# Kernel tuning notes

Hardware: AMD Instinct MI355X
Metric: run time of the kernel (lower is better)

Reference implementation:

```python
import jax, jax.numpy as jnp
import numpy as np

B, T, D = 8, 2048, 1024
H, N = 8, 32  # n_heads, n_state


def _xavier(key, shape, fan_in, fan_out):
    lim = float(np.sqrt(6.0 / (fan_in + fan_out)))
    return jax.random.uniform(key, shape, jnp.float32, -lim, lim)


def setup_inputs() -> dict:
    key = jax.random.key(0)
    ks = jax.random.split(key, 8)
    x = jax.random.normal(ks[0], (B, T, D), jnp.float32)
    W_in = _xavier(ks[1], (D, D), D, D)                    # in_proj.weight [d_inner, dim]
    # per-head xavier on [n_state, d_inner] slices -> limit sqrt(6/(N+D))
    W_k = _xavier(ks[2], (H * N, D), N, D)
    W_v = _xavier(ks[3], (H * N, D), N, D)
    W_q = _xavier(ks[4], (H * N, D), N, D)
    W_beta = _xavier(ks[5], (H * N, D), N, D)
    b_beta = jnp.full((H, N), 2.0, jnp.float32)            # init_beta_bias
    W_out = _xavier(ks[6], (D, H * N), H * N, D)           # out_proj.weight [dim, H*n]
    return {"x": x, "W_in": W_in, "W_k": W_k, "W_v": W_v, "W_q": W_q,
            "W_beta": W_beta, "b_beta": b_beta, "W_out": W_out}


def reference(x, W_in, W_k, W_v, W_q, W_beta, b_beta, W_out):
    b, t, d = x.shape
    h, n = b_beta.shape
    # in_proj + SiLU (use_conv=False)
    xp = jax.nn.silu(jnp.einsum('btd,ed->bte', x, W_in))   # [B,T,D_inner]
    def proj(W):  # -> [T,B,H,N]
        return jnp.einsum('btd,md->btm', xp, W).reshape(b, t, h, n).transpose(1, 0, 2, 3)
    k_all = proj(W_k)
    v_all = proj(W_v)
    q_all = proj(W_q)
    beta_all = jax.nn.sigmoid(proj(W_beta) + b_beta)       # [T,B,H,N]

    S0 = jnp.zeros((b, h, n, n), x.dtype)

    def step(S, inp):
        k, v, q, beta = inp                                 # each [B,H,N]
        kn = k / (jnp.linalg.norm(k, axis=-1, keepdims=True) + 1e-6)
        retrieved = jnp.einsum('bhij,bhj->bhi', S, kn)
        delta = v - retrieved
        S = jnp.tanh(beta[..., None] * S + delta[..., None] * kn[..., None, :])
        Sq = jnp.einsum('bhij,bhj->bhi', S, q)
        out = Sq * jax.nn.silu(Sq)                          # [B,H,N]
        return S, out

    S_final, outs = jax.lax.scan(step, S0, (k_all, v_all, q_all, beta_all))
    cell_out = outs.transpose(1, 0, 2, 3).reshape(b, t, h * n)  # [B,T,H*N]
    y = jnp.einsum('btm,dm->btd', cell_out, W_out)          # out_proj, no bias
    return y, S_final
```

## Files before the change

### kernel.cpp

```cpp
#include <hip/hip_runtime.h>
#include <hip/hip_bf16.h>

#define TT 2048
#define BB 8
#define HH 8
#define NNS 32
#define MM (BB * TT)
#define CH 16

typedef __attribute__((ext_vector_type(8))) short short8;
typedef __attribute__((ext_vector_type(4))) float f32x4;

__device__ __forceinline__ float bf2f(ushort u) {
    return __uint_as_float(((unsigned)u) << 16);
}
__device__ __forceinline__ ushort f2bf(float f) {
    unsigned x = __float_as_uint(f);
    unsigned r = (x + 0x7fffu + ((x >> 16) & 1u)) >> 16;
    return (ushort)r;
}
__device__ __forceinline__ float sigmoidf_fast(float x) {
    float e = __builtin_amdgcn_exp2f(x * -1.4426950408889634f);
    return __builtin_amdgcn_rcpf(1.0f + e);
}
__device__ __forceinline__ float tanhf_fast(float x) {
    float e = __builtin_amdgcn_exp2f(x * 2.8853900817779268f);
    return fmaf(-2.0f, __builtin_amdgcn_rcpf(e + 1.0f), 1.0f);
}

template<int CTRL>
__device__ __forceinline__ float dpp_add(float x) {
    int y = __builtin_amdgcn_update_dpp(0, __float_as_int(x), CTRL, 0xF, 0xF, true);
    return x + __int_as_float(y);
}
__device__ __forceinline__ float red16(float x) {
    x = dpp_add<0xB1>(x);
    x = dpp_add<0x4E>(x);
    x = dpp_add<0x124>(x);
    x = dpp_add<0x128>(x);
    return x;
}

__device__ __forceinline__ void split8(const float4& x0, const float4& x1,
                                       ushort* __restrict__ h, ushort* __restrict__ l) {
    float xs[8] = {x0.x, x0.y, x0.z, x0.w, x1.x, x1.y, x1.z, x1.w};
#pragma unroll
    for (int i = 0; i < 8; ++i) {
        ushort hh = f2bf(xs[i]);
        h[i] = hh;
        l[i] = f2bf(xs[i] - bf2f(hh));
    }
}

__global__ __launch_bounds__(256) void conv_x_kernel(
    const float* __restrict__ src, ushort* __restrict__ hi, ushort* __restrict__ lo)
{
    size_t e = ((size_t)blockIdx.x * 256 + threadIdx.x) * 8;
    float4 x0 = *reinterpret_cast<const float4*>(src + e);
    float4 x1 = *reinterpret_cast<const float4*>(src + e + 4);
    ushort h[8], l[8];
    split8(x0, x1, h, l);
    *reinterpret_cast<uint4*>(hi + e) = *reinterpret_cast<const uint4*>(h);
    *reinterpret_cast<uint4*>(lo + e) = *reinterpret_cast<const uint4*>(l);
}

__global__ __launch_bounds__(256) void conv_w_kernel(
    const float* __restrict__ Wi, const float* __restrict__ Wk,
    const float* __restrict__ Wv, const float* __restrict__ Wq,
    const float* __restrict__ Wb, const float* __restrict__ Wo,
    ushort* __restrict__ W1h, ushort* __restrict__ W1l,
    ushort* __restrict__ W2h, ushort* __restrict__ W2l,
    ushort* __restrict__ W3h)
{
    size_t e = ((size_t)blockIdx.x * 256 + threadIdx.x) * 8;
    const float* s;
    ushort* dh; ushort* dl; size_t doff; bool dolo = true;
    if (e < 1048576) {
        s = Wi + e; dh = W1h; dl = W1l; doff = e;
    } else if (e < 2097152) {
        size_t u = e - 1048576;
        int wi = (int)(u >> 18);
        const float* sp = (wi == 0) ? Wk : (wi == 1) ? Wv : (wi == 2) ? Wq : Wb;
        s = sp + (u & 262143); dh = W2h; dl = W2l; doff = u;
    } else {
        size_t u = e - 2097152;
        s = Wo + u; dh = W3h; dl = nullptr; doff = u; dolo = false;
    }
    float4 x0 = *reinterpret_cast<const float4*>(s);
    float4 x1 = *reinterpret_cast<const float4*>(s + 4);
    ushort h[8], l[8];
    split8(x0, x1, h, l);
    *reinterpret_cast<uint4*>(dh + doff) = *reinterpret_cast<const uint4*>(h);
    if (dolo)
        *reinterpret_cast<uint4*>(dl + doff) = *reinterpret_cast<const uint4*>(l);
}

template<int ACT>
__global__ __launch_bounds__(256, 2) void gemm_planes(
    const ushort* __restrict__ Ah_g, const ushort* __restrict__ Al_g,
    const ushort* __restrict__ Wh_g, const ushort* __restrict__ Wl_g,
    const float* __restrict__ bbeta,
    ushort* __restrict__ Ch, ushort* __restrict__ Cl,
    float* __restrict__ Cf, int M, int N, int K)
{
    __shared__ __align__(16) ushort sAh[2][128][40], sAl[2][128][40];
    __shared__ __align__(16) ushort sWh[2][128][40], sWl[2][128][40];
    const int n0 = blockIdx.x * 128;
    const int m0 = blockIdx.y * 128;
    const int t  = threadIdx.x;
    const int wave = t >> 6, lane = t & 63;
    const int lr = lane & 15, lq = lane >> 4;
    const int wm = wave >> 1, wn = wave & 1;

    const int sr = t >> 1;
    const int sc = (t & 1) * 16;

    const ushort* pAh = Ah_g + (size_t)(m0 + sr) * K + sc;
    const ushort* pAl = Al_g + (size_t)(m0 + sr) * K + sc;
    const ushort* pWh = Wh_g + (size_t)(n0 + sr) * K + sc;
    const ushort* pWl = Wl_g + (size_t)(n0 + sr) * K + sc;

    f32x4 acc[4][4];
#pragma unroll
    for (int mi = 0; mi < 4; ++mi)
#pragma unroll
        for (int ni = 0; ni < 4; ++ni) acc[mi][ni] = (f32x4){0.f, 0.f, 0.f, 0.f};

    const int NK = K >> 5;

    {
        uint4 a0 = *reinterpret_cast<const uint4*>(pAh);
        uint4 a1 = *reinterpret_cast<const uint4*>(pAh + 8);
        uint4 l0 = *reinterpret_cast<const uint4*>(pAl);
        uint4 l1 = *reinterpret_cast<const uint4*>(pAl + 8);
        uint4 w0 = *reinterpret_cast<const uint4*>(pWh);
        uint4 w1 = *reinterpret_cast<const uint4*>(pWh + 8);
        uint4 u0 = *reinterpret_cast<const uint4*>(pWl);
        uint4 u1 = *reinterpret_cast<const uint4*>(pWl + 8);
        *reinterpret_cast<uint4*>(&sAh[0][sr][sc])     = a0;
        *reinterpret_cast<uint4*>(&sAh[0][sr][sc + 8]) = a1;
        *reinterpret_cast<uint4*>(&sAl[0][sr][sc])     = l0;
        *reinterpret_cast<uint4*>(&sAl[0][sr][sc + 8]) = l1;
        *reinterpret_cast<uint4*>(&sWh[0][sr][sc])     = w0;
        *reinterpret_cast<uint4*>(&sWh[0][sr][sc + 8]) = w1;
        *reinterpret_cast<uint4*>(&sWl[0][sr][sc])     = u0;
        *reinterpret_cast<uint4*>(&sWl[0][sr][sc + 8]) = u1;
    }
    __syncthreads();

    for (int ks = 0; ks < NK; ++ks) {
        const int cur = ks & 1;
        uint4 a0, a1, l0, l1, w0, w1, u0, u1;
        const bool pf = (ks + 1 < NK);
        if (pf) {
            const int off = (ks + 1) << 5;
            a0 = *reinterpret_cast<const uint4*>(pAh + off);
            a1 = *reinterpret_cast<const uint4*>(pAh + off + 8);
            l0 = *reinterpret_cast<const uint4*>(pAl + off);
            l1 = *reinterpret_cast<const uint4*>(pAl + off + 8);
            w0 = *reinterpret_cast<const uint4*>(pWh + off);
            w1 = *reinterpret_cast<const uint4*>(pWh + off + 8);
            u0 = *reinterpret_cast<const uint4*>(pWl + off);
            u1 = *reinterpret_cast<const uint4*>(pWl + off + 8);
        }
        short8 ah[4], al[4], wh[4], wl[4];
#pragma unroll
        for (int mi = 0; mi < 4; ++mi) {
            ah[mi] = *reinterpret_cast<const short8*>(&sAh[cur][wm * 64 + mi * 16 + lr][lq * 8]);
            al[mi] = *reinterpret_cast<const short8*>(&sAl[cur][wm * 64 + mi * 16 + lr][lq * 8]);
        }
#pragma unroll
        for (int ni = 0; ni < 4; ++ni) {
            wh[ni] = *reinterpret_cast<const short8*>(&sWh[cur][wn * 64 + ni * 16 + lr][lq * 8]);
            wl[ni] = *reinterpret_cast<const short8*>(&sWl[cur][wn * 64 + ni * 16 + lr][lq * 8]);
        }
#pragma unroll
        for (int mi = 0; mi < 4; ++mi) {
#pragma unroll
            for (int ni = 0; ni < 4; ++ni) {
                acc[mi][ni] = __builtin_amdgcn_mfma_f32_16x16x32_bf16(ah[mi], wh[ni], acc[mi][ni], 0, 0, 0);
                acc[mi][ni] = __builtin_amdgcn_mfma_f32_16x16x32_bf16(ah[mi], wl[ni], acc[mi][ni], 0, 0, 0);
                acc[mi][ni] = __builtin_amdgcn_mfma_f32_16x16x32_bf16(al[mi], wh[ni], acc[mi][ni], 0, 0, 0);
            }
        }
        if (pf) {
            const int nxt = cur ^ 1;
            *reinterpret_cast<uint4*>(&sAh[nxt][sr][sc])     = a0;
            *reinterpret_cast<uint4*>(&sAh[nxt][sr][sc + 8]) = a1;
            *reinterpret_cast<uint4*>(&sAl[nxt][sr][sc])     = l0;
            *reinterpret_cast<uint4*>(&sAl[nxt][sr][sc + 8]) = l1;
            *reinterpret_cast<uint4*>(&sWh[nxt][sr][sc])     = w0;
            *reinterpret_cast<uint4*>(&sWh[nxt][sr][sc + 8]) = w1;
            *reinterpret_cast<uint4*>(&sWl[nxt][sr][sc])     = u0;
            *reinterpret_cast<uint4*>(&sWl[nxt][sr][sc + 8]) = u1;
        }
        __syncthreads();
    }

#pragma unroll
    for (int mi = 0; mi < 4; ++mi) {
#pragma unroll
        for (int ni = 0; ni < 4; ++ni) {
#pragma unroll
            for (int r2 = 0; r2 < 4; ++r2) {
                int mg = m0 + wm * 64 + mi * 16 + lq * 4 + r2;
                int ng = n0 + wn * 64 + ni * 16 + lr;
                float v = acc[mi][ni][r2];
                if (ACT == 1) {
                    v = v * sigmoidf_fast(v);
                    ushort h = f2bf(v);
                    ushort lo_ = f2bf(v - bf2f(h));
                    Ch[(size_t)mg * N + ng] = h;
                    Cl[(size_t)mg * N + ng] = lo_;
                } else {
                    if (ACT == 2 && ng >= 768) v = sigmoidf_fast(v + bbeta[ng - 768]);
                    Cf[(size_t)mg * N + ng] = v;
                }
            }
        }
    }
}

__global__ __launch_bounds__(256, 2) void gemm_cell(
    const ushort* __restrict__ A, const ushort* __restrict__ Wh_g,
    float* __restrict__ C, int M, int N, int K)
{
    __shared__ __align__(16) ushort sA[2][128][40];
    __shared__ __align__(16) ushort sW[2][128][40];
    const int n0 = blockIdx.x * 128;
    const int m0 = blockIdx.y * 128;
    const int t  = threadIdx.x;
    const int wave = t >> 6, lane = t & 63;
    const int lr = lane & 15, lq = lane >> 4;
    const int wm = wave >> 1, wn = wave & 1;
    const int sr = t >> 1;
    const int sc = (t & 1) * 16;

    const ushort* pA = A    + (size_t)(m0 + sr) * K + sc;
    const ushort* pW = Wh_g + (size_t)(n0 + sr) * K + sc;

    f32x4 acc[4][4];
#pragma unroll
    for (int mi = 0; mi < 4; ++mi)
#pragma unroll
        for (int ni = 0; ni < 4; ++ni) acc[mi][ni] = (f32x4){0.f, 0.f, 0.f, 0.f};

    const int NK = K >> 5;
    {
        uint4 a0 = *reinterpret_cast<const uint4*>(pA);
        uint4 a1 = *reinterpret_cast<const uint4*>(pA + 8);
        uint4 w0 = *reinterpret_cast<const uint4*>(pW);
        uint4 w1 = *reinterpret_cast<const uint4*>(pW + 8);
        *reinterpret_cast<uint4*>(&sA[0][sr][sc])     = a0;
        *reinterpret_cast<uint4*>(&sA[0][sr][sc + 8]) = a1;
        *reinterpret_cast<uint4*>(&sW[0][sr][sc])     = w0;
        *reinterpret_cast<uint4*>(&sW[0][sr][sc + 8]) = w1;
    }
    __syncthreads();

    for (int ks = 0; ks < NK; ++ks) {
        const int cur = ks & 1;
        uint4 a0, a1, w0, w1;
        const bool pf = (ks + 1 < NK);
        if (pf) {
            const int off = (ks + 1) << 5;
            a0 = *reinterpret_cast<const uint4*>(pA + off);
            a1 = *reinterpret_cast<const uint4*>(pA + off + 8);
            w0 = *reinterpret_cast<const uint4*>(pW + off);
            w1 = *reinterpret_cast<const uint4*>(pW + off + 8);
        }
        short8 af[4], wf[4];
#pragma unroll
        for (int mi = 0; mi < 4; ++mi)
            af[mi] = *reinterpret_cast<const short8*>(&sA[cur][wm * 64 + mi * 16 + lr][lq * 8]);
#pragma unroll
        for (int ni = 0; ni < 4; ++ni)
            wf[ni] = *reinterpret_cast<const short8*>(&sW[cur][wn * 64 + ni * 16 + lr][lq * 8]);
#pragma unroll
        for (int mi = 0; mi < 4; ++mi)
#pragma unroll
            for (int ni = 0; ni < 4; ++ni)
                acc[mi][ni] = __builtin_amdgcn_mfma_f32_16x16x32_bf16(af[mi], wf[ni], acc[mi][ni], 0, 0, 0);
        if (pf) {
            const int nxt = cur ^ 1;
            *reinterpret_cast<uint4*>(&sA[nxt][sr][sc])     = a0;
            *reinterpret_cast<uint4*>(&sA[nxt][sr][sc + 8]) = a1;
            *reinterpret_cast<uint4*>(&sW[nxt][sr][sc])     = w0;
            *reinterpret_cast<uint4*>(&sW[nxt][sr][sc + 8]) = w1;
        }
        __syncthreads();
    }

#pragma unroll
    for (int mi = 0; mi < 4; ++mi) {
#pragma unroll
        for (int ni = 0; ni < 4; ++ni) {
#pragma unroll
            for (int r2 = 0; r2 < 4; ++r2) {
                int mg = m0 + wm * 64 + mi * 16 + lq * 4 + r2;
                int ng = n0 + wn * 64 + ni * 16 + lr;
                C[(size_t)mg * N + ng] = acc[mi][ni][r2];
            }
        }
    }
}

__global__ __launch_bounds__(256) void kn_kernel(
    const float* __restrict__ P, float* __restrict__ KN)
{
    int idx = blockIdx.x * 256 + threadIdx.x;
    int col = idx & 255;
    int bt  = idx >> 8;
    float k = P[(size_t)bt * 1024 + col];
    float ks = k * k;
    ks += __shfl_xor(ks, 1, 32);  ks += __shfl_xor(ks, 2, 32);
    ks += __shfl_xor(ks, 4, 32);  ks += __shfl_xor(ks, 8, 32);
    ks += __shfl_xor(ks, 16, 32);
    KN[idx] = k * __builtin_amdgcn_rcpf(sqrtf(ks) + 1e-6f);
}

__device__ __forceinline__ void lds_load8(
    float (&K_)[CH][32], float (&Q_)[CH][32], float (&VB)[CH][8],
    int base, int l, int iw,
    float (&k0)[8], float (&k1)[8], float (&q0)[8], float (&q1)[8],
    float (&vv)[8], float (&bb)[8])
{
#pragma unroll
    for (int u = 0; u < 8; ++u) {
        k0[u] = K_[base + u][l];  k1[u] = K_[base + u][l + 16];
        q0[u] = Q_[base + u][l];  q1[u] = Q_[base + u][l + 16];
        vv[u] = VB[base + u][iw]; bb[u] = VB[base + u][iw + 4];
    }
}

__device__ __forceinline__ void steps8(
    float (&k0)[8], float (&k1)[8], float (&q0)[8], float (&q1)[8],
    float (&vv)[8], float (&bb)[8],
    float& S0, float& S1, float (&sqp)[8])
{
#pragma unroll
    for (int u = 0; u < 8; ++u) {
        float p = red16(fmaf(S0, k0[u], S1 * k1[u]));
        float delta = vv[u] - p;
        S0 = tanhf_fast(fmaf(bb[u], S0, delta * k0[u]));
        S1 = tanhf_fast(fmaf(bb[u], S1, delta * k1[u]));
        sqp[u] = fmaf(S0, q0[u], S1 * q1[u]);
    }
}

__device__ __forceinline__ void flush8(
    float (&sqp)[8], ushort* __restrict__ cell, size_t crow, int l)
{
    float r0 = red16(sqp[0]), r1 = red16(sqp[1]);
    float r2 = red16(sqp[2]), r3 = red16(sqp[3]);
    float r4 = red16(sqp[4]), r5 = red16(sqp[5]);
    float r6 = red16(sqp[6]), r7 = red16(sqp[7]);
    if (l < 8) {
        float s01 = (l & 1) ? r1 : r0;
        float s23 = (l & 1) ? r3 : r2;
        float s45 = (l & 1) ? r5 : r4;
        float s67 = (l & 1) ? r7 : r6;
        float a03 = (l & 2) ? s23 : s01;
        float a47 = (l & 2) ? s67 : s45;
        float sel = (l & 4) ? a47 : a03;
        float o = sel * sel * sigmoidf_fast(sel);
        cell[crow + (size_t)l * 256] = f2bf(o);
    }
}

template<int DO_STAGE>
__device__ __forceinline__ void scan_chunk16(
    float (&K_)[CH][32], float (&Q_)[CH][32], float (&VB)[CH][8],
    float (&NK)[CH][32], float (&NQ)[CH][32], float (&NVB)[CH][8],
    const float*& gkn, const float*& gq, const float*& gv, const float*& gb,
    float (&k0A)[8], float (&k1A)[8], float (&q0A)[8], float (&q1A)[8],
    float (&vvA)[8], float (&bbA)[8],
    float (&k0B)[8], float (&k1B)[8], float (&q0B)[8], float (&q1B)[8],
    float (&vvB)[8], float (&bbB)[8],
    float& S0, float& S1, float (&sqp)[8],
    ushort* __restrict__ cell, size_t crow, int l, int iw, int j)
{
    float4 Lk0, Lk1, Lq0, Lq1;
    float Lv = 0.f, Lb = 0.f;
    if (DO_STAGE) {
        Lk0 = *reinterpret_cast<const float4*>(gkn);
        Lk1 = *reinterpret_cast<const float4*>(gkn + 8 * 256);
        Lq0 = *reinterpret_cast<const float4*>(gq);
        Lq1 = *reinterpret_cast<const float4*>(gq + 8 * 1024);
        Lv  = *gv;
        Lb  = *gb;
        gkn += CH * 256; gq += CH * 1024; gv += CH * 1024; gb += CH * 1024;
    }
    lds_load8(K_, Q_, VB, 8, l, iw, k0B, k1B, q0B, q1B, vvB, bbB);
    steps8(k0A, k1A, q0A, q1A, vvA, bbA, S0, S1, sqp);
    flush8(sqp, cell, crow, l);
    if (DO_STAGE) {
        *reinterpret_cast<float4*>(&NK[j >> 3][(j & 7) * 4]) = Lk0;
        *reinterpret_cast<float4*>(&NK[8 + (j >> 3)][(j & 7) * 4]) = Lk1;
        *reinterpret_cast<float4*>(&NQ[j >> 3][(j & 7) * 4]) = Lq0;
        *reinterpret_cast<float4*>(&NQ[8 + (j >> 3)][(j & 7) * 4]) = Lq1;
        NVB[j >> 2][j & 3] = Lv;
        NVB[j >> 2][4 + (j & 3)] = Lb;
        lds_load8(NK, NQ, NVB, 0, l, iw, k0A, k1A, q0A, q1A, vvA, bbA);
    }
    steps8(k0B, k1B, q0B, q1B, vvB, bbB, S0, S1, sqp);
    flush8(sqp, cell, crow + (size_t)8 * 256, l);
}

__global__ __launch_bounds__(64, 1) void scan_kernel(
    const float* __restrict__ P,
    const float* __restrict__ KN,
    ushort* __restrict__ cell,
    float* __restrict__ Sout)
{
    const int b    = blockIdx.x & 7;
    const int r    = blockIdx.x >> 3;
    const int h    = r & 7;
    const int quad = r >> 3;
    const int j    = threadIdx.x;
    const int l    = j & 15;
    const int iw   = j >> 4;
    const int i    = quad * 4 + iw;

    __shared__ __align__(16) float sK0[CH][32], sK1[CH][32];
    __shared__ __align__(16) float sQ0[CH][32], sQ1[CH][32];
    __shared__ __align__(16) float sVB0[CH][8], sVB1[CH][8];

    const size_t bt0 = (size_t)b * TT;
    const float* gkn = KN + (bt0 + (j >> 3)) * 256 + h * 32 + (j & 7) * 4;
    const float* gq  = P  + (bt0 + (j >> 3)) * 1024 + 512 + h * 32 + (j & 7) * 4;
    const float* gv  = P  + (bt0 + (j >> 2)) * 1024 + 256 + h * 32 + quad * 4 + (j & 3);
    const float* gb  = P  + (bt0 + (j >> 2)) * 1024 + 768 + h * 32 + quad * 4 + (j & 3);

    float k0A[8], k1A[8], q0A[8], q1A[8], vvA[8], bbA[8];
    float k0B[8], k1B[8], q0B[8], q1B[8], vvB[8], bbB[8];
    float sqp[8];
    float S0 = 0.f, S1 = 0.f;
    const size_t cb = (size_t)b * TT * 256 + h * 32 + i;

    {
        float4 K0v = *reinterpret_cast<const float4*>(gkn);
        float4 K1v = *reinterpret_cast<const float4*>(gkn + 8 * 256);
        float4 Q0v = *reinterpret_cast<const float4*>(gq);
        float4 Q1v = *reinterpret_cast<const float4*>(gq + 8 * 1024);
        float v0 = *gv, b0 = *gb;
        gkn += CH * 256; gq += CH * 1024; gv += CH * 1024; gb += CH * 1024;
        *reinterpret_cast<float4*>(&sK0[j >> 3][(j & 7) * 4]) = K0v;
        *reinterpret_cast<float4*>(&sK0[8 + (j >> 3)][(j & 7) * 4]) = K1v;
        *reinterpret_cast<float4*>(&sQ0[j >> 3][(j & 7) * 4]) = Q0v;
        *reinterpret_cast<float4*>(&sQ0[8 + (j >> 3)][(j & 7) * 4]) = Q1v;
        sVB0[j >> 2][j & 3] = v0;
        sVB0[j >> 2][4 + (j & 3)] = b0;
    }
    lds_load8(sK0, sQ0, sVB0, 0, l, iw, k0A, k1A, q0A, q1A, vvA, bbA);

    size_t crow = cb;
    for (int c = 0; c < 63; ++c) {
        scan_chunk16<1>(sK0, sQ0, sVB0, sK1, sQ1, sVB1,
                        gkn, gq, gv, gb,
                        k0A, k1A, q0A, q1A, vvA, bbA,
                        k0B, k1B, q0B, q1B, vvB, bbB,
                        S0, S1, sqp, cell, crow, l, iw, j);
        crow += (size_t)CH * 256;
        scan_chunk16<1>(sK1, sQ1, sVB1, sK0, sQ0, sVB0,
                        gkn, gq, gv, gb,
                        k0A, k1A, q0A, q1A, vvA, bbA,
                        k0B, k1B, q0B, q1B, vvB, bbB,
                        S0, S1, sqp, cell, crow, l, iw, j);
        crow += (size_t)CH * 256;
    }
    scan_chunk16<1>(sK0, sQ0, sVB0, sK1, sQ1, sVB1,
                    gkn, gq, gv, gb,
                    k0A, k1A, q0A, q1A, vvA, bbA,
                    k0B, k1B, q0B, q1B, vvB, bbB,
                    S0, S1, sqp, cell, crow, l, iw, j);
    crow += (size_t)CH * 256;
    scan_chunk16<0>(sK1, sQ1, sVB1, sK0, sQ0, sVB0,
                    gkn, gq, gv, gb,
                    k0A, k1A, q0A, q1A, vvA, bbA,
                    k0B, k1B, q0B, q1B, vvB, bbB,
                    S0, S1, sqp, cell, crow, l, iw, j);

    float* so = Sout + (((size_t)(b * HH + h)) * NNS + i) * NNS;
    so[l] = S0;
    so[l + 16] = S1;
}

extern "C" void kernel_launch(void* const* d_in, const int* in_sizes, int n_in,
                              void* d_out, int out_size, void* d_ws, size_t ws_size,
                              hipStream_t stream) {
    const float* x     = (const float*)d_in[0];
    const float* W_in  = (const float*)d_in[1];
    const float* W_k   = (const float*)d_in[2];
    const float* W_v   = (const float*)d_in[3];
    const float* W_q   = (const float*)d_in[4];
    const float* W_b   = (const float*)d_in[5];
    const float* b_b   = (const float*)d_in[6];
    const float* W_out = (const float*)d_in[7];
    float* out = (float*)d_out;

    const int M = MM;
    float* f = (float*)d_ws;
    float*  P    = f;
    ushort* Xh   = (ushort*)f;
    ushort* Xl   = Xh + (size_t)M * 1024;
    ushort* xpH  = (ushort*)(f + (size_t)M * 1024);
    ushort* xpL  = xpH + (size_t)M * 1024;
    float*  KN   = f + (size_t)2 * M * 1024;
    ushort* cell = (ushort*)(KN + (size_t)M * 256);
    ushort* wb   = cell + (size_t)M * 256;
    ushort* W1h = wb;
    ushort* W1l = W1h + 1048576;
    ushort* W2h = W1l + 1048576;
    ushort* W2l = W2h + 1048576;
    ushort* W3h = W2l + 1048576;

    dim3 blk(256);
    dim3 g1(1024 / 128, M / 128);

    conv_x_kernel<<<dim3((M * 1024) / (8 * 256)), blk, 0, stream>>>(x, Xh, Xl);
    conv_w_kernel<<<dim3(2359296 / (8 * 256)), blk, 0, stream>>>(
        W_in, W_k, W_v, W_q, W_b, W_out, W1h, W1l, W2h, W2l, W3h);
    gemm_planes<1><<<g1, blk, 0, stream>>>(Xh, Xl, W1h, W1l, b_b,
                                           xpH, xpL, nullptr, M, 1024, 1024);
    gemm_planes<2><<<g1, blk, 0, stream>>>(xpH, xpL, W2h, W2l, b_b,
                                           nullptr, nullptr, P, M, 1024, 1024);
    kn_kernel<<<dim3((M * 256) / 256), blk, 0, stream>>>(P, KN);
    scan_kernel<<<dim3(512), dim3(64), 0, stream>>>(P, KN, cell, out + (size_t)M * 1024);
    gemm_cell<<<g1, blk, 0, stream>>>(cell, W3h, out, M, 1024, 256);
}
```

Baseline: 593.7 us.

## Stage GEMM tiles via direct global-to-LDS loads with block swizzle

Both bf16 MFMA GEMM kernels now load tiles straight from global memory into LDS with global_load_lds, replacing the register-staged, double-buffered copies. LDS tiles drop to a single unpadded buffer, and launch bounds rise to allow more resident blocks per CU. A block-index swizzle reorders tile assignment to improve L2 reuse of shared A and W tiles. In exchange, the loop loses explicit load/compute overlap, adds a second barrier per k-step, and the unpadded 64-byte rows may cause LDS bank conflicts. The swizzle also hardcodes an 8-wide, 128-tall grid.

```diff
diff --git a/kernel.cpp b/kernel.cpp
--- a/kernel.cpp
+++ b/kernel.cpp
@@ -26,6 +26,12 @@
 __device__ __forceinline__ float tanhf_fast(float x) {
     float e = __builtin_amdgcn_exp2f(x * 2.8853900817779268f);
     return fmaf(-2.0f, __builtin_amdgcn_rcpf(e + 1.0f), 1.0f);
+}
+
+__device__ __forceinline__ void gl16(const void* g, void* l) {
+    auto gp = (const __attribute__((address_space(1))) unsigned int*)g;
+    auto lp = (__attribute__((address_space(3))) unsigned int*)l;
+    __builtin_amdgcn_global_load_lds(gp, lp, 16, 0, 0);
 }
 
 template<int CTRL>
@@ -96,29 +102,41 @@
 }
 
 template<int ACT>
-__global__ __launch_bounds__(256, 2) void gemm_planes(
+__global__ __launch_bounds__(256, 3) void gemm_planes(
     const ushort* __restrict__ Ah_g, const ushort* __restrict__ Al_g,
     const ushort* __restrict__ Wh_g, const ushort* __restrict__ Wl_g,
     const float* __restrict__ bbeta,
     ushort* __restrict__ Ch, ushort* __restrict__ Cl,
     float* __restrict__ Cf, int M, int N, int K)
 {
-    __shared__ __align__(16) ushort sAh[2][128][40], sAl[2][128][40];
-    __shared__ __align__(16) ushort sWh[2][128][40], sWl[2][128][40];
-    const int n0 = blockIdx.x * 128;
-    const int m0 = blockIdx.y * 128;
-    const int t  = threadIdx.x;
+    __shared__ __align__(16) ushort sAh[128][32], sAl[128][32];
+    __shared__ __align__(16) ushort sWh[128][32], sWl[128][32];
+    const int t = threadIdx.x;
     const int wave = t >> 6, lane = t & 63;
     const int lr = lane & 15, lq = lane >> 4;
     const int wm = wave >> 1, wn = wave & 1;
 
-    const int sr = t >> 1;
-    const int sc = (t & 1) * 16;
-
-    const ushort* pAh = Ah_g + (size_t)(m0 + sr) * K + sc;
-    const ushort* pAl = Al_g + (size_t)(m0 + sr) * K + sc;
-    const ushort* pWh = Wh_g + (size_t)(n0 + sr) * K + sc;
-    const ushort* pWl = Wl_g + (size_t)(n0 + sr) * K + sc;
+    const int bid = blockIdx.y * 8 + blockIdx.x;
+    const int swz = (bid & 7) * 128 + (bid >> 3);
+    const int n0 = (swz & 7) * 128;
+    const int m0 = (swz >> 3) * 128;
+
+    const int rs0 = wave * 32 + (lane >> 2);
+    const int rs1 = rs0 + 16;
+    const int ce  = (lane & 3) * 8;
+    const ushort* gA0h = Ah_g + (size_t)(m0 + rs0) * K + ce;
+    const ushort* gA1h = Ah_g + (size_t)(m0 + rs1) * K + ce;
+    const ushort* gA0l = Al_g + (size_t)(m0 + rs0) * K + ce;
+    const ushort* gA1l = Al_g + (size_t)(m0 + rs1) * K + ce;
+    const ushort* gW0h = Wh_g + (size_t)(n0 + rs0) * K + ce;
+    const ushort* gW1h = Wh_g + (size_t)(n0 + rs1) * K + ce;
+    const ushort* gW0l = Wl_g + (size_t)(n0 + rs0) * K + ce;
+    const ushort* gW1l = Wl_g + (size_t)(n0 + rs1) * K + ce;
+    const int lb = wave * 2048 + lane * 16;
+    char* LAh = (char*)&sAh[0][0];
+    char* LAl = (char*)&sAl[0][0];
+    char* LWh = (char*)&sWh[0][0];
+    char* LWl = (char*)&sWl[0][0];
 
     f32x4 acc[4][4];
 #pragma unroll
@@ -127,52 +145,24 @@
         for (int ni = 0; ni < 4; ++ni) acc[mi][ni] = (f32x4){0.f, 0.f, 0.f, 0.f};
 
     const int NK = K >> 5;
-
-    {
-        uint4 a0 = *reinterpret_cast<const uint4*>(pAh);
-        uint4 a1 = *reinterpret_cast<const uint4*>(pAh + 8);
-        uint4 l0 = *reinterpret_cast<const uint4*>(pAl);
-        uint4 l1 = *reinterpret_cast<const uint4*>(pAl + 8);
-        uint4 w0 = *reinterpret_cast<const uint4*>(pWh);
-        uint4 w1 = *reinterpret_cast<const uint4*>(pWh + 8);
-        uint4 u0 = *reinterpret_cast<const uint4*>(pWl);
-        uint4 u1 = *reinterpret_cast<const uint4*>(pWl + 8);
-        *reinterpret_cast<uint4*>(&sAh[0][sr][sc])     = a0;
-        *reinterpret_cast<uint4*>(&sAh[0][sr][sc + 8]) = a1;
-        *reinterpret_cast<uint4*>(&sAl[0][sr][sc])     = l0;
-        *reinterpret_cast<uint4*>(&sAl[0][sr][sc + 8]) = l1;
-        *reinterpret_cast<uint4*>(&sWh[0][sr][sc])     = w0;
-        *reinterpret_cast<uint4*>(&sWh[0][sr][sc + 8]) = w1;
-        *reinterpret_cast<uint4*>(&sWl[0][sr][sc])     = u0;
-        *reinterpret_cast<uint4*>(&sWl[0][sr][sc + 8]) = u1;
-    }
-    __syncthreads();
-
     for (int ks = 0; ks < NK; ++ks) {
-        const int cur = ks & 1;
-        uint4 a0, a1, l0, l1, w0, w1, u0, u1;
-        const bool pf = (ks + 1 < NK);
-        if (pf) {
-            const int off = (ks + 1) << 5;
-            a0 = *reinterpret_cast<const uint4*>(pAh + off);
-            a1 = *reinterpret_cast<const uint4*>(pAh + off + 8);
-            l0 = *reinterpret_cast<const uint4*>(pAl + off);
-            l1 = *reinterpret_cast<const uint4*>(pAl + off + 8);
-            w0 = *reinterpret_cast<const uint4*>(pWh + off);
-            w1 = *reinterpret_cast<const uint4*>(pWh + off + 8);
-            u0 = *reinterpret_cast<const uint4*>(pWl + off);
-            u1 = *reinterpret_cast<const uint4*>(pWl + off + 8);
+        const int k0 = ks << 5;
+        __syncthreads();
+        gl16(gA0h + k0, LAh + lb);  gl16(gA1h + k0, LAh + lb + 1024);
+        gl16(gA0l + k0, LAl + lb);  gl16(gA1l + k0, LAl + lb + 1024);
+        gl16(gW0h + k0, LWh + lb);  gl16(gW1h + k0, LWh + lb + 1024);
+        gl16(gW0l + k0, LWl + lb);  gl16(gW1l + k0, LWl + lb + 1024);
+        __syncthreads();
+        short8 ah[4], al[4], wh[4], wl[4];
+#pragma unroll
+        for (int mi = 0; mi < 4; ++mi) {
+            ah[mi] = *reinterpret_cast<const short8*>(&sAh[wm * 64 + mi * 16 + lr][lq * 8]);
+            al[mi] = *reinterpret_cast<const short8*>(&sAl[wm * 64 + mi * 16 + lr][lq * 8]);
         }
-        short8 ah[4], al[4], wh[4], wl[4];
-#pragma unroll
-        for (int mi = 0; mi < 4; ++mi) {
-            ah[mi] = *reinterpret_cast<const short8*>(&sAh[cur][wm * 64 + mi * 16 + lr][lq * 8]);
-            al[mi] = *reinterpret_cast<const short8*>(&sAl[cur][wm * 64 + mi * 16 + lr][lq * 8]);
-        }
 #pragma unroll
         for (int ni = 0; ni < 4; ++ni) {
-            wh[ni] = *reinterpret_cast<const short8*>(&sWh[cur][wn * 64 + ni * 16 + lr][lq * 8]);
-            wl[ni] = *reinterpret_cast<const short8*>(&sWl[cur][wn * 64 + ni * 16 + lr][lq * 8]);
+            wh[ni] = *reinterpret_cast<const short8*>(&sWh[wn * 64 + ni * 16 + lr][lq * 8]);
+            wl[ni] = *reinterpret_cast<const short8*>(&sWl[wn * 64 + ni * 16 + lr][lq * 8]);
         }
 #pragma unroll
         for (int mi = 0; mi < 4; ++mi) {
@@ -183,18 +173,6 @@
                 acc[mi][ni] = __builtin_amdgcn_mfma_f32_16x16x32_bf16(al[mi], wh[ni], acc[mi][ni], 0, 0, 0);
             }
         }
-        if (pf) {
-            const int nxt = cur ^ 1;
-            *reinterpret_cast<uint4*>(&sAh[nxt][sr][sc])     = a0;
-            *reinterpret_cast<uint4*>(&sAh[nxt][sr][sc + 8]) = a1;
-            *reinterpret_cast<uint4*>(&sAl[nxt][sr][sc])     = l0;
-            *reinterpret_cast<uint4*>(&sAl[nxt][sr][sc + 8]) = l1;
-            *reinterpret_cast<uint4*>(&sWh[nxt][sr][sc])     = w0;
-            *reinterpret_cast<uint4*>(&sWh[nxt][sr][sc + 8]) = w1;
-            *reinterpret_cast<uint4*>(&sWl[nxt][sr][sc])     = u0;
-            *reinterpret_cast<uint4*>(&sWl[nxt][sr][sc + 8]) = u1;
-        }
-        __syncthreads();
     }
 
 #pragma unroll
@@ -221,23 +199,32 @@
     }
 }
 
-__global__ __launch_bounds__(256, 2) void gemm_cell(
+__global__ __launch_bounds__(256, 4) void gemm_cell(
     const ushort* __restrict__ A, const ushort* __restrict__ Wh_g,
     float* __restrict__ C, int M, int N, int K)
 {
-    __shared__ __align__(16) ushort sA[2][128][40];
-    __shared__ __align__(16) ushort sW[2][128][40];
-    const int n0 = blockIdx.x * 128;
-    const int m0 = blockIdx.y * 128;
-    const int t  = threadIdx.x;
+    __shared__ __align__(16) ushort sA[128][32];
+    __shared__ __align__(16) ushort sW[128][32];
+    const int t = threadIdx.x;
     const int wave = t >> 6, lane = t & 63;
     const int lr = lane & 15, lq = lane >> 4;
     const int wm = wave >> 1, wn = wave & 1;
-    const int sr = t >> 1;
-    const int sc = (t & 1) * 16;
-
-    const ushort* pA = A    + (size_t)(m0 + sr) * K + sc;
-    const ushort* pW = Wh_g + (size_t)(n0 + sr) * K + sc;
+
+    const int bid = blockIdx.y * 8 + blockIdx.x;
+    const int swz = (bid & 7) * 128 + (bid >> 3);
+    const int n0 = (swz & 7) * 128;
+    const int m0 = (swz >> 3) * 128;
+
+    const int rs0 = wave * 32 + (lane >> 2);
+    const int rs1 = rs0 + 16;
+    const int ce  = (lane & 3) * 8;
+    const ushort* gA0 = A    + (size_t)(m0 + rs0) * K + ce;
+    const ushort* gA1 = A    + (size_t)(m0 + rs1) * K + ce;
+    const ushort* gW0 = Wh_g + (size_t)(n0 + rs0) * K + ce;
+    const ushort* gW1 = Wh_g + (size_t)(n0 + rs1) * K + ce;
+    const int lb = wave * 2048 + lane * 16;
+    char* LA = (char*)&sA[0][0];
+    char* LW = (char*)&sW[0][0];
 
     f32x4 acc[4][4];
 #pragma unroll
@@ -246,49 +233,24 @@
         for (int ni = 0; ni < 4; ++ni) acc[mi][ni] = (f32x4){0.f, 0.f, 0.f, 0.f};
 
     const int NK = K >> 5;
-    {
-        uint4 a0 = *reinterpret_cast<const uint4*>(pA);
-        uint4 a1 = *reinterpret_cast<const uint4*>(pA + 8);
-        uint4 w0 = *reinterpret_cast<const uint4*>(pW);
-        uint4 w1 = *reinterpret_cast<const uint4*>(pW + 8);
-        *reinterpret_cast<uint4*>(&sA[0][sr][sc])     = a0;
-        *reinterpret_cast<uint4*>(&sA[0][sr][sc + 8]) = a1;
-        *reinterpret_cast<uint4*>(&sW[0][sr][sc])     = w0;
-        *reinterpret_cast<uint4*>(&sW[0][sr][sc + 8]) = w1;
-    }
-    __syncthreads();
-
     for (int ks = 0; ks < NK; ++ks) {
-        const int cur = ks & 1;
-        uint4 a0, a1, w0, w1;
-        const bool pf = (ks + 1 < NK);
-        if (pf) {
-            const int off = (ks + 1) << 5;
-            a0 = *reinterpret_cast<const uint4*>(pA + off);
-            a1 = *reinterpret_cast<const uint4*>(pA + off + 8);
-            w0 = *reinterpret_cast<const uint4*>(pW + off);
-            w1 = *reinterpret_cast<const uint4*>(pW + off + 8);
-        }
+        const int k0 = ks << 5;
+        __syncthreads();
+        gl16(gA0 + k0, LA + lb);  gl16(gA1 + k0, LA + lb + 1024);
+        gl16(gW0 + k0, LW + lb);  gl16(gW1 + k0, LW + lb + 1024);
+        __syncthreads();
         short8 af[4], wf[4];
 #pragma unroll
         for (int mi = 0; mi < 4; ++mi)
-            af[mi] = *reinterpret_cast<const short8*>(&sA[cur][wm * 64 + mi * 16 + lr][lq * 8]);
+            af[mi] = *reinterpret_cast<const short8*>(&sA[wm * 64 + mi * 16 + lr][lq * 8]);
 #pragma unroll
         for (int ni = 0; ni < 4; ++ni)
-            wf[ni] = *reinterpret_cast<const short8*>(&sW[cur][wn * 64 + ni * 16 + lr][lq * 8]);
+            wf[ni] = *reinterpret_cast<const short8*>(&sW[wn * 64 + ni * 16 + lr][lq * 8]);
 #pragma unroll
         for (int mi = 0; mi < 4; ++mi)
 #pragma unroll
             for (int ni = 0; ni < 4; ++ni)
                 acc[mi][ni] = __builtin_amdgcn_mfma_f32_16x16x32_bf16(af[mi], wf[ni], acc[mi][ni], 0, 0, 0);
-        if (pf) {
-            const int nxt = cur ^ 1;
-            *reinterpret_cast<uint4*>(&sA[nxt][sr][sc])     = a0;
-            *reinterpret_cast<uint4*>(&sA[nxt][sr][sc + 8]) = a1;
-            *reinterpret_cast<uint4*>(&sW[nxt][sr][sc])     = w0;
-            *reinterpret_cast<uint4*>(&sW[nxt][sr][sc + 8]) = w1;
-        }
-        __syncthreads();
     }
 
 #pragma unroll
```

After: 569.1 us. 4.1% less time.
